# Kernel optimization log

Hardware: AMD Instinct MI355X
Metric: run time of the kernel (lower is better)

The kernel has to match this reference:

```python
import jax, jax.numpy as jnp
import numpy as np

N = 100000   # nodes
E = 100000   # hyperedges
M = 1600000  # incidences
IN_C = 128
HID = 128
OUT_C = 64
L = 2
EPS = 1e-5


def _layer_norm(x, g, b):
    m = jnp.mean(x, axis=-1, keepdims=True)
    v = jnp.mean((x - m) ** 2, axis=-1, keepdims=True)
    return (x - m) * jax.lax.rsqrt(v + EPS) * g + b


def setup_inputs() -> dict:
    key = jax.random.key(0)
    ks = jax.random.split(key, 16)
    s_in = 1.0 / np.sqrt(IN_C)
    s_h = 1.0 / np.sqrt(HID)
    return {
        "x": jax.random.normal(ks[0], (N, IN_C), jnp.float32),
        "x_e": jax.random.normal(ks[1], (E, IN_C), jnp.float32),
        "edge_index": jax.random.randint(ks[2], (2, M), 0, N, jnp.int32),
        "in_norm_g": jnp.ones((IN_C,), jnp.float32),
        "in_norm_b": jnp.zeros((IN_C,), jnp.float32),
        "in_proj_W": jax.random.normal(ks[3], (IN_C, HID), jnp.float32) * s_in,
        "in_proj_b": jnp.zeros((HID,), jnp.float32),
        "norm_g": jnp.ones((L, HID), jnp.float32),
        "norm_b": jnp.zeros((L, HID), jnp.float32),
        "conv_W": jax.random.normal(ks[4], (L, HID, HID), jnp.float32) * s_h,
        "conv_b": jnp.zeros((L, HID), jnp.float32),
        "lin_W": jax.random.normal(ks[5], (HID, OUT_C), jnp.float32) * s_h,
        "lin_b": jnp.zeros((OUT_C,), jnp.float32),
    }


def reference(x, x_e, edge_index, in_norm_g, in_norm_b, in_proj_W, in_proj_b,
              norm_g, norm_b, conv_W, conv_b, lin_W, lin_b):
    src, dst = edge_index[0], edge_index[1]  # node ids, hyperedge ids
    h = _layer_norm(x, in_norm_g, in_norm_b)
    h = jax.nn.leaky_relu(h @ in_proj_W + in_proj_b)  # dropout = identity (eval)

    # HypergraphConv degree normalizers (hyperedge_weight = 1)
    ones = jnp.ones((M,), h.dtype)
    degD = jax.ops.segment_sum(ones, src, num_segments=N)
    D = jnp.where(degD > 0, 1.0 / degD, 0.0)          # [N]
    degB = jax.ops.segment_sum(ones, dst, num_segments=E)
    B = jnp.where(degB > 0, 1.0 / degB, 0.0)          # [E]

    for i in range(L):
        hn = _layer_norm(h, norm_g[i], norm_b[i])
        xw = hn @ conv_W[i]                            # [N, HID]
        # node -> hyperedge: sum_j B[e] * xw[j]
        he = jax.ops.segment_sum(B[dst][:, None] * xw[src], dst, num_segments=E)
        # hyperedge -> node: sum_e D[n] * he[e]
        h2 = jax.ops.segment_sum(D[src][:, None] * he[dst], src, num_segments=N)
        h = jax.nn.leaky_relu(h2 + conv_b[i])

    # MinAggregation: segment-min of gathered node features per hyperedge
    agg = jax.ops.segment_min(h[src], dst, num_segments=E)  # [E, HID]
    return agg @ lin_W + lin_b                              # [E, OUT_C]
```

## Files before the change

kernel.cpp:

```cpp
#include <hip/hip_runtime.h>

#define NN 100000
#define NE 100000
#define MI 1600000
#define HID 128
#define OUTC 64
#define LSLOPE 0.01f
#define EPSV 1e-5f
#define ADJ_STRIDE 48
#define BUILD_PASSES 6
#define BUILD_WIN ((NN + BUILD_PASSES - 1) / BUILD_PASSES)

typedef unsigned short us;
typedef __attribute__((ext_vector_type(4))) unsigned short us4;
typedef __attribute__((ext_vector_type(8))) short short8;
typedef __attribute__((ext_vector_type(16))) float f32x16;

__device__ __forceinline__ float bf2f(us h) {
    return __uint_as_float(((unsigned)h) << 16);
}
__device__ __forceinline__ us f2bf(float f) {
    unsigned u = __float_as_uint(f);
    return (us)((u + 0x7FFFu + ((u >> 16) & 1u)) >> 16);
}

__global__ void build_win_kernel(const int* __restrict__ ei,
                                 int* __restrict__ cntE, int* __restrict__ cntN,
                                 int* __restrict__ adjE, int* __restrict__ adjN,
                                 int lo, int hi) {
    int m = blockIdx.x * blockDim.x + threadIdx.x;
    if (m >= MI) return;
    int s = ei[m], d = ei[MI + m];
    if (d >= lo && d < hi) {
        int p = atomicAdd(&cntE[d], 1);
        if (p < ADJ_STRIDE) adjE[d * ADJ_STRIDE + p] = s;
    }
    if (s >= lo && s < hi) {
        int p = atomicAdd(&cntN[s], 1);
        if (p < ADJ_STRIDE) adjN[s * ADJ_STRIDE + p] = d;
    }
}

__global__ void recip2_kernel(const int* __restrict__ cntE, const int* __restrict__ cntN,
                              float* __restrict__ B, float* __restrict__ D) {
    int i = blockIdx.x * blockDim.x + threadIdx.x;
    if (i < NE) {
        int d = cntE[i]; B[i] = d > 0 ? 1.0f / (float)d : 0.0f;
    } else if (i < NE + NN) {
        int j = i - NE;
        int d = cntN[j]; D[j] = d > 0 ? 1.0f / (float)d : 0.0f;
    }
}

__global__ void wprep_kernel(const float* __restrict__ in_W, const float* __restrict__ conv_W,
                             const float* __restrict__ lin_W,
                             us* __restrict__ wt_in, us* __restrict__ wt_c0,
                             us* __restrict__ wt_c1, us* __restrict__ wt_lin) {
    int idx = blockIdx.x * blockDim.x + threadIdx.x;
    if (idx < 49152) {
        int mat = idx >> 14, r = idx & 16383;
        const float* src = mat == 0 ? in_W : (mat == 1 ? conv_W : conv_W + 16384);
        us* dst = mat == 0 ? wt_in : (mat == 1 ? wt_c0 : wt_c1);
        int n = r >> 7, k = r & 127;
        dst[r] = f2bf(src[k * 128 + n]);
    } else if (idx < 57344) {
        int r = idx - 49152;
        int n = r >> 7, k = r & 127;
        float v = lin_W[k * 64 + n];
        us h = f2bf(v);
        wt_lin[r] = h;
        wt_lin[8192 + r] = f2bf(v - bf2f(h));
    }
}

template <int MODE>
__global__ __launch_bounds__(256) void gather_kernel(
    const int* __restrict__ cnt, const int* __restrict__ adj,
    const us* __restrict__ src, const float* __restrict__ scale,
    const float* __restrict__ bias, us* __restrict__ dst, int R)
{
    int g = threadIdx.x >> 5;
    int lane = threadIdx.x & 31;
    int r = blockIdx.x * 8 + g;
    if (r >= R) return;
    int n = cnt[r]; n = n < ADJ_STRIDE ? n : ADJ_STRIDE;
    const int* arow = adj + (size_t)r * ADJ_STRIDE;
    float ax, ay, az, aw;
    if (MODE == 2) { ax = ay = az = aw = INFINITY; }
    else           { ax = ay = az = aw = 0.f; }
    const us* base = src + lane * 4;
    int j = 0;
    for (; j + 7 < n; j += 8) {
        us4 v0 = *(const us4*)(base + (size_t)arow[j]     * HID);
        us4 v1 = *(const us4*)(base + (size_t)arow[j + 1] * HID);
        us4 v2 = *(const us4*)(base + (size_t)arow[j + 2] * HID);
        us4 v3 = *(const us4*)(base + (size_t)arow[j + 3] * HID);
        us4 v4 = *(const us4*)(base + (size_t)arow[j + 4] * HID);
        us4 v5 = *(const us4*)(base + (size_t)arow[j + 5] * HID);
        us4 v6 = *(const us4*)(base + (size_t)arow[j + 6] * HID);
        us4 v7 = *(const us4*)(base + (size_t)arow[j + 7] * HID);
        if (MODE == 2) {
            ax = fminf(ax, fminf(fminf(fminf(bf2f(v0.x), bf2f(v1.x)), fminf(bf2f(v2.x), bf2f(v3.x))),
                                 fminf(fminf(bf2f(v4.x), bf2f(v5.x)), fminf(bf2f(v6.x), bf2f(v7.x)))));
            ay = fminf(ay, fminf(fminf(fminf(bf2f(v0.y), bf2f(v1.y)), fminf(bf2f(v2.y), bf2f(v3.y))),
                                 fminf(fminf(bf2f(v4.y), bf2f(v5.y)), fminf(bf2f(v6.y), bf2f(v7.y)))));
            az = fminf(az, fminf(fminf(fminf(bf2f(v0.z), bf2f(v1.z)), fminf(bf2f(v2.z), bf2f(v3.z))),
                                 fminf(fminf(bf2f(v4.z), bf2f(v5.z)), fminf(bf2f(v6.z), bf2f(v7.z)))));
            aw = fminf(aw, fminf(fminf(fminf(bf2f(v0.w), bf2f(v1.w)), fminf(bf2f(v2.w), bf2f(v3.w))),
                                 fminf(fminf(bf2f(v4.w), bf2f(v5.w)), fminf(bf2f(v6.w), bf2f(v7.w)))));
        } else {
            ax += ((bf2f(v0.x) + bf2f(v1.x)) + (bf2f(v2.x) + bf2f(v3.x)))
                + ((bf2f(v4.x) + bf2f(v5.x)) + (bf2f(v6.x) + bf2f(v7.x)));
            ay += ((bf2f(v0.y) + bf2f(v1.y)) + (bf2f(v2.y) + bf2f(v3.y)))
                + ((bf2f(v4.y) + bf2f(v5.y)) + (bf2f(v6.y) + bf2f(v7.y)));
            az += ((bf2f(v0.z) + bf2f(v1.z)) + (bf2f(v2.z) + bf2f(v3.z)))
                + ((bf2f(v4.z) + bf2f(v5.z)) + (bf2f(v6.z) + bf2f(v7.z)));
            aw += ((bf2f(v0.w) + bf2f(v1.w)) + (bf2f(v2.w) + bf2f(v3.w)))
                + ((bf2f(v4.w) + bf2f(v5.w)) + (bf2f(v6.w) + bf2f(v7.w)));
        }
    }
    for (; j + 1 < n; j += 2) {
        us4 v0 = *(const us4*)(base + (size_t)arow[j]     * HID);
        us4 v1 = *(const us4*)(base + (size_t)arow[j + 1] * HID);
        if (MODE == 2) {
            ax = fminf(ax, fminf(bf2f(v0.x), bf2f(v1.x)));
            ay = fminf(ay, fminf(bf2f(v0.y), bf2f(v1.y)));
            az = fminf(az, fminf(bf2f(v0.z), bf2f(v1.z)));
            aw = fminf(aw, fminf(bf2f(v0.w), bf2f(v1.w)));
        } else {
            ax += bf2f(v0.x) + bf2f(v1.x);
            ay += bf2f(v0.y) + bf2f(v1.y);
            az += bf2f(v0.z) + bf2f(v1.z);
            aw += bf2f(v0.w) + bf2f(v1.w);
        }
    }
    if (j < n) {
        us4 v0 = *(const us4*)(base + (size_t)arow[j] * HID);
        if (MODE == 2) {
            ax = fminf(ax, bf2f(v0.x)); ay = fminf(ay, bf2f(v0.y));
            az = fminf(az, bf2f(v0.z)); aw = fminf(aw, bf2f(v0.w));
        } else {
            ax += bf2f(v0.x); ay += bf2f(v0.y); az += bf2f(v0.z); aw += bf2f(v0.w);
        }
    }
    if (MODE == 0) {
        float s = scale[r];
        ax *= s; ay *= s; az *= s; aw *= s;
    } else if (MODE == 1) {
        float s = scale[r];
        float4 b = *(const float4*)(bias + lane * 4);
        float x;
        x = s * ax + b.x; ax = x > 0.f ? x : LSLOPE * x;
        x = s * ay + b.y; ay = x > 0.f ? x : LSLOPE * x;
        x = s * az + b.z; az = x > 0.f ? x : LSLOPE * x;
        x = s * aw + b.w; aw = x > 0.f ? x : LSLOPE * x;
    }
    us4 o;
    o.x = f2bf(ax); o.y = f2bf(ay); o.z = f2bf(az); o.w = f2bf(aw);
    *(us4*)(dst + (size_t)r * HID + lane * 4) = o;
}

template <int NC, bool ABF16, bool OBF16, bool SPLIT>
__global__ __launch_bounds__(512) void mfma_gemm_kernel(
    const void* __restrict__ Av, const float* __restrict__ ln_g, const float* __restrict__ ln_b,
    const us* __restrict__ WT, const float* __restrict__ bias,
    void* __restrict__ outv, int R, int flags)
{
    constexpr int SA = 136;
    constexpr int NW = (SPLIT ? 2 : 1) * NC;
    constexpr int CT = NC / 64;
    __shared__ us As[128 * SA];
    __shared__ us Ws[NW * SA];
    __shared__ float red_s[512];
    __shared__ float red_q[512];
    __shared__ float r_mean[128];
    __shared__ float r_rstd[128];

    const int t = threadIdx.x;
    const int row0 = blockIdx.x * 128;

    constexpr int WUS4 = NW * 128 / 4;
    #pragma unroll
    for (int i = t; i < WUS4; i += 512) {
        us4 w = ((const us4*)WT)[i];
        int nrow = i >> 5, k4 = i & 31;
        *(us4*)(Ws + nrow * SA + k4 * 4) = w;
    }

    {
        const int r = t >> 2, sub = t & 3;
        const int gr = row0 + r;
        float v[32];
        if (gr < R) {
            if (ABF16) {
                const us* ap = (const us*)Av + (size_t)gr * 128 + sub * 32;
                #pragma unroll
                for (int j4 = 0; j4 < 8; ++j4) {
                    us4 x4 = *(const us4*)(ap + j4 * 4);
                    v[j4 * 4 + 0] = bf2f(x4.x); v[j4 * 4 + 1] = bf2f(x4.y);
                    v[j4 * 4 + 2] = bf2f(x4.z); v[j4 * 4 + 3] = bf2f(x4.w);
                }
            } else {
                const float* ap = (const float*)Av + (size_t)gr * 128 + sub * 32;
                #pragma unroll
                for (int j4 = 0; j4 < 8; ++j4) {
                    float4 f4 = *(const float4*)(ap + j4 * 4);
                    v[j4 * 4 + 0] = f4.x; v[j4 * 4 + 1] = f4.y;
                    v[j4 * 4 + 2] = f4.z; v[j4 * 4 + 3] = f4.w;
                }
            }
        } else {
            #pragma unroll
            for (int j = 0; j < 32; ++j) v[j] = 0.f;
        }
        if (flags & 1) {
            float s = 0.f, q = 0.f;
            #pragma unroll
            for (int j = 0; j < 32; ++j) { s += v[j]; q += v[j] * v[j]; }
            red_s[t] = s; red_q[t] = q;
            __syncthreads();
            if (t < 128) {
                float ss = red_s[t * 4] + red_s[t * 4 + 1] + red_s[t * 4 + 2] + red_s[t * 4 + 3];
                float qq = red_q[t * 4] + red_q[t * 4 + 1] + red_q[t * 4 + 2] + red_q[t * 4 + 3];
                float mu = ss * (1.0f / 128.0f);
                float var = qq * (1.0f / 128.0f) - mu * mu;
                r_mean[t] = mu;
                r_rstd[t] = rsqrtf(var + EPSV);
            }
            __syncthreads();
            float mu = r_mean[r], rs = r_rstd[r];
            #pragma unroll
            for (int j4 = 0; j4 < 8; ++j4) {
                float4 g4 = *(const float4*)(ln_g + sub * 32 + j4 * 4);
                float4 b4 = *(const float4*)(ln_b + sub * 32 + j4 * 4);
                v[j4 * 4 + 0] = (v[j4 * 4 + 0] - mu) * rs * g4.x + b4.x;
                v[j4 * 4 + 1] = (v[j4 * 4 + 1] - mu) * rs * g4.y + b4.y;
                v[j4 * 4 + 2] = (v[j4 * 4 + 2] - mu) * rs * g4.z + b4.z;
                v[j4 * 4 + 3] = (v[j4 * 4 + 3] - mu) * rs * g4.w + b4.w;
            }
        }
        #pragma unroll
        for (int j4 = 0; j4 < 8; ++j4) {
            us4 o;
            o.x = f2bf(v[j4 * 4 + 0]); o.y = f2bf(v[j4 * 4 + 1]);
            o.z = f2bf(v[j4 * 4 + 2]); o.w = f2bf(v[j4 * 4 + 3]);
            *(us4*)(As + r * SA + sub * 32 + j4 * 4) = o;
        }
    }
    __syncthreads();

    const int lane = t & 63;
    const int wave = t >> 6;
    const int wr = (wave & 3) * 32;
    const int wc = (wave >> 2) * (NC / 2);
    const int m = lane & 31;
    const int half = lane >> 5;
    const us* a_base = As + (wr + m) * SA + half * 8;

    f32x16 acc[CT];
    #pragma unroll
    for (int ct = 0; ct < CT; ++ct) acc[ct] = (f32x16)(0.0f);

    #pragma unroll
    for (int ks = 0; ks < 8; ++ks) {
        short8 a = *(const short8*)(a_base + ks * 16);
        #pragma unroll
        for (int ct = 0; ct < CT; ++ct) {
            const us* b_base = Ws + (wc + ct * 32 + m) * SA + half * 8 + ks * 16;
            short8 b = *(const short8*)b_base;
            acc[ct] = __builtin_amdgcn_mfma_f32_32x32x16_bf16(a, b, acc[ct], 0, 0, 0);
            if (SPLIT) {
                short8 bl = *(const short8*)(b_base + (size_t)NC * SA);
                acc[ct] = __builtin_amdgcn_mfma_f32_32x32x16_bf16(a, bl, acc[ct], 0, 0, 0);
            }
        }
    }

    #pragma unroll
    for (int ct = 0; ct < CT; ++ct) {
        int gc = wc + ct * 32 + m;
        float bv = bias ? bias[gc] : 0.f;
        #pragma unroll
        for (int reg = 0; reg < 16; ++reg) {
            int rloc = (reg & 3) + 8 * (reg >> 2) + 4 * half;
            int gr = row0 + wr + rloc;
            if (gr < R) {
                float y = acc[ct][reg] + bv;
                if (flags & 4) y = y > 0.f ? y : LSLOPE * y;
                if (OBF16) ((us*)outv)[(size_t)gr * NC + gc] = f2bf(y);
                else       ((float*)outv)[(size_t)gr * NC + gc] = y;
            }
        }
    }
}

extern "C" void kernel_launch(void* const* d_in, const int* in_sizes, int n_in,
                              void* d_out, int out_size, void* d_ws, size_t ws_size,
                              hipStream_t stream) {
    const float* x      = (const float*)d_in[0];
    const int*   ei     = (const int*)d_in[2];
    const float* in_g   = (const float*)d_in[3];
    const float* in_b   = (const float*)d_in[4];
    const float* in_W   = (const float*)d_in[5];
    const float* in_pb  = (const float*)d_in[6];
    const float* norm_g = (const float*)d_in[7];
    const float* norm_b = (const float*)d_in[8];
    const float* conv_W = (const float*)d_in[9];
    const float* conv_b = (const float*)d_in[10];
    const float* lin_W  = (const float*)d_in[11];
    const float* lin_b  = (const float*)d_in[12];
    float* out = (float*)d_out;

    us* h_bf   = (us*)d_ws;
    us* xw_bf  = h_bf  + (size_t)NN * HID;
    us* he_bf  = xw_bf + (size_t)NN * HID;
    us* agg_bf = he_bf + (size_t)NE * HID;
    float* D    = (float*)(agg_bf + (size_t)NE * HID);
    float* B    = D + NN;
    int* cntE   = (int*)(B + NE);
    int* cntN   = cntE + NE;
    int* adjE   = cntN + NN;
    int* adjN   = adjE + (size_t)NE * ADJ_STRIDE;
    us* wt_in  = (us*)(adjN + (size_t)NN * ADJ_STRIDE);
    us* wt_c0  = wt_in + 128 * 128;
    us* wt_c1  = wt_c0 + 128 * 128;
    us* wt_lin = wt_c1 + 128 * 128;

    hipMemsetAsync(cntE, 0, (size_t)(NN + NE) * sizeof(int), stream);
    for (int p = 0; p < BUILD_PASSES; ++p) {
        int lo = p * BUILD_WIN;
        int hi = lo + BUILD_WIN < NN ? lo + BUILD_WIN : NN;
        build_win_kernel<<<(MI + 255) / 256, 256, 0, stream>>>(ei, cntE, cntN, adjE, adjN, lo, hi);
    }
    recip2_kernel<<<(NN + NE + 255) / 256, 256, 0, stream>>>(cntE, cntN, B, D);

    wprep_kernel<<<(57344 + 255) / 256, 256, 0, stream>>>(
        in_W, conv_W, lin_W, wt_in, wt_c0, wt_c1, wt_lin);

    mfma_gemm_kernel<HID, false, true, false><<<(NN + 127) / 128, 512, 0, stream>>>(
        x, in_g, in_b, wt_in, in_pb, h_bf, NN, 1 | 4);

    for (int i = 0; i < 2; ++i) {
        mfma_gemm_kernel<HID, true, true, false><<<(NN + 127) / 128, 512, 0, stream>>>(
            h_bf, norm_g + i * HID, norm_b + i * HID, i ? wt_c1 : wt_c0,
            nullptr, xw_bf, NN, 1);
        gather_kernel<0><<<(NE + 7) / 8, 256, 0, stream>>>(cntE, adjE, xw_bf, B, nullptr, he_bf, NE);
        gather_kernel<1><<<(NN + 7) / 8, 256, 0, stream>>>(cntN, adjN, he_bf, D, conv_b + i * HID, h_bf, NN);
    }

    gather_kernel<2><<<(NE + 7) / 8, 256, 0, stream>>>(cntE, adjE, h_bf, nullptr, nullptr, agg_bf, NE);

    mfma_gemm_kernel<OUTC, true, false, true><<<(NE + 127) / 128, 512, 0, stream>>>(
        agg_bf, nullptr, nullptr, wt_lin, lin_b, out, NE, 0);
}
```

Baseline: 757.8 us.

## Widen gather loads to 16 bytes and fold build passes into one launch

Gather kernels now use 16 lanes per row, each loading 8 bf16 values (16 bytes) per neighbour instead of 4. This halves the number of load instructions and doubles the rows handled per block. The windowed adjacency build goes from 6 separate launches to one grid covering 10 windows, and the reciprocal-degree and weight-prep kernels are merged into one launch. Running all windows in a single grid loses the ordering between windows, which may raise atomic contention and weaken the locality that windowing was meant to give.

After: 745.8 us (median of 2 runs). Within noise of the previous version (-1.6%).

```diff
diff --git a/kernel.cpp b/kernel.cpp
--- a/kernel.cpp
+++ b/kernel.cpp
@@ -8,11 +8,13 @@
 #define LSLOPE 0.01f
 #define EPSV 1e-5f
 #define ADJ_STRIDE 48
-#define BUILD_PASSES 6
+#define BUILD_PASSES 10
 #define BUILD_WIN ((NN + BUILD_PASSES - 1) / BUILD_PASSES)
+#define BUILD_NB ((MI + 255) / 256)
 
 typedef unsigned short us;
 typedef __attribute__((ext_vector_type(4))) unsigned short us4;
+typedef __attribute__((ext_vector_type(8))) unsigned short us8;
 typedef __attribute__((ext_vector_type(8))) short short8;
 typedef __attribute__((ext_vector_type(16))) float f32x16;
 
@@ -24,12 +26,14 @@
     return (us)((u + 0x7FFFu + ((u >> 16) & 1u)) >> 16);
 }
 
-__global__ void build_win_kernel(const int* __restrict__ ei,
+__global__ void build_all_kernel(const int* __restrict__ ei,
                                  int* __restrict__ cntE, int* __restrict__ cntN,
-                                 int* __restrict__ adjE, int* __restrict__ adjN,
-                                 int lo, int hi) {
-    int m = blockIdx.x * blockDim.x + threadIdx.x;
+                                 int* __restrict__ adjE, int* __restrict__ adjN) {
+    int pass = blockIdx.x / BUILD_NB;
+    int m = (blockIdx.x - pass * BUILD_NB) * 256 + threadIdx.x;
     if (m >= MI) return;
+    int lo = pass * BUILD_WIN;
+    int hi = lo + BUILD_WIN < NN ? lo + BUILD_WIN : NN;
     int s = ei[m], d = ei[MI + m];
     if (d >= lo && d < hi) {
         int p = atomicAdd(&cntE[d], 1);
@@ -41,35 +45,34 @@
     }
 }
 
-__global__ void recip2_kernel(const int* __restrict__ cntE, const int* __restrict__ cntN,
-                              float* __restrict__ B, float* __restrict__ D) {
+__global__ void prep_kernel(const int* __restrict__ cntE, const int* __restrict__ cntN,
+                            float* __restrict__ B, float* __restrict__ D,
+                            const float* __restrict__ in_W, const float* __restrict__ conv_W,
+                            const float* __restrict__ lin_W,
+                            us* __restrict__ wt_in, us* __restrict__ wt_c0,
+                            us* __restrict__ wt_c1, us* __restrict__ wt_lin) {
     int i = blockIdx.x * blockDim.x + threadIdx.x;
     if (i < NE) {
         int d = cntE[i]; B[i] = d > 0 ? 1.0f / (float)d : 0.0f;
     } else if (i < NE + NN) {
         int j = i - NE;
         int d = cntN[j]; D[j] = d > 0 ? 1.0f / (float)d : 0.0f;
-    }
-}
-
-__global__ void wprep_kernel(const float* __restrict__ in_W, const float* __restrict__ conv_W,
-                             const float* __restrict__ lin_W,
-                             us* __restrict__ wt_in, us* __restrict__ wt_c0,
-                             us* __restrict__ wt_c1, us* __restrict__ wt_lin) {
-    int idx = blockIdx.x * blockDim.x + threadIdx.x;
-    if (idx < 49152) {
-        int mat = idx >> 14, r = idx & 16383;
-        const float* src = mat == 0 ? in_W : (mat == 1 ? conv_W : conv_W + 16384);
-        us* dst = mat == 0 ? wt_in : (mat == 1 ? wt_c0 : wt_c1);
-        int n = r >> 7, k = r & 127;
-        dst[r] = f2bf(src[k * 128 + n]);
-    } else if (idx < 57344) {
-        int r = idx - 49152;
-        int n = r >> 7, k = r & 127;
-        float v = lin_W[k * 64 + n];
-        us h = f2bf(v);
-        wt_lin[r] = h;
-        wt_lin[8192 + r] = f2bf(v - bf2f(h));
+    } else {
+        int idx = i - (NE + NN);
+        if (idx < 49152) {
+            int mat = idx >> 14, r = idx & 16383;
+            const float* src = mat == 0 ? in_W : (mat == 1 ? conv_W : conv_W + 16384);
+            us* dst = mat == 0 ? wt_in : (mat == 1 ? wt_c0 : wt_c1);
+            int n = r >> 7, k = r & 127;
+            dst[r] = f2bf(src[k * 128 + n]);
+        } else if (idx < 57344) {
+            int r = idx - 49152;
+            int n = r >> 7, k = r & 127;
+            float v = lin_W[k * 64 + n];
+            us h = f2bf(v);
+            wt_lin[r] = h;
+            wt_lin[8192 + r] = f2bf(v - bf2f(h));
+        }
     }
 }
 
@@ -79,85 +82,58 @@
     const us* __restrict__ src, const float* __restrict__ scale,
     const float* __restrict__ bias, us* __restrict__ dst, int R)
 {
-    int g = threadIdx.x >> 5;
-    int lane = threadIdx.x & 31;
-    int r = blockIdx.x * 8 + g;
+    const int q = threadIdx.x >> 4;
+    const int lane = threadIdx.x & 15;
+    const int r = blockIdx.x * 16 + q;
     if (r >= R) return;
     int n = cnt[r]; n = n < ADJ_STRIDE ? n : ADJ_STRIDE;
     const int* arow = adj + (size_t)r * ADJ_STRIDE;
-    float ax, ay, az, aw;
-    if (MODE == 2) { ax = ay = az = aw = INFINITY; }
-    else           { ax = ay = az = aw = 0.f; }
-    const us* base = src + lane * 4;
+    float a[8];
+    #pragma unroll
+    for (int k = 0; k < 8; ++k) a[k] = (MODE == 2) ? INFINITY : 0.f;
+    const us* base = src + lane * 8;
     int j = 0;
     for (; j + 7 < n; j += 8) {
-        us4 v0 = *(const us4*)(base + (size_t)arow[j]     * HID);
-        us4 v1 = *(const us4*)(base + (size_t)arow[j + 1] * HID);
-        us4 v2 = *(const us4*)(base + (size_t)arow[j + 2] * HID);
-        us4 v3 = *(const us4*)(base + (size_t)arow[j + 3] * HID);
-        us4 v4 = *(const us4*)(base + (size_t)arow[j + 4] * HID);
-        us4 v5 = *(const us4*)(base + (size_t)arow[j + 5] * HID);
-        us4 v6 = *(const us4*)(base + (size_t)arow[j + 6] * HID);
-        us4 v7 = *(const us4*)(base + (size_t)arow[j + 7] * HID);
-        if (MODE == 2) {
-            ax = fminf(ax, fminf(fminf(fminf(bf2f(v0.x), bf2f(v1.x)), fminf(bf2f(v2.x), bf2f(v3.x))),
-                                 fminf(fminf(bf2f(v4.x), bf2f(v5.x)), fminf(bf2f(v6.x), bf2f(v7.x)))));
-            ay = fminf(ay, fminf(fminf(fminf(bf2f(v0.y), bf2f(v1.y)), fminf(bf2f(v2.y), bf2f(v3.y))),
-                                 fminf(fminf(bf2f(v4.y), bf2f(v5.y)), fminf(bf2f(v6.y), bf2f(v7.y)))));
-            az = fminf(az, fminf(fminf(fminf(bf2f(v0.z), bf2f(v1.z)), fminf(bf2f(v2.z), bf2f(v3.z))),
-                                 fminf(fminf(bf2f(v4.z), bf2f(v5.z)), fminf(bf2f(v6.z), bf2f(v7.z)))));
-            aw = fminf(aw, fminf(fminf(fminf(bf2f(v0.w), bf2f(v1.w)), fminf(bf2f(v2.w), bf2f(v3.w))),
-                                 fminf(fminf(bf2f(v4.w), bf2f(v5.w)), fminf(bf2f(v6.w), bf2f(v7.w)))));
-        } else {
-            ax += ((bf2f(v0.x) + bf2f(v1.x)) + (bf2f(v2.x) + bf2f(v3.x)))
-                + ((bf2f(v4.x) + bf2f(v5.x)) + (bf2f(v6.x) + bf2f(v7.x)));
-            ay += ((bf2f(v0.y) + bf2f(v1.y)) + (bf2f(v2.y) + bf2f(v3.y)))
-                + ((bf2f(v4.y) + bf2f(v5.y)) + (bf2f(v6.y) + bf2f(v7.y)));
-            az += ((bf2f(v0.z) + bf2f(v1.z)) + (bf2f(v2.z) + bf2f(v3.z)))
-                + ((bf2f(v4.z) + bf2f(v5.z)) + (bf2f(v6.z) + bf2f(v7.z)));
-            aw += ((bf2f(v0.w) + bf2f(v1.w)) + (bf2f(v2.w) + bf2f(v3.w)))
-                + ((bf2f(v4.w) + bf2f(v5.w)) + (bf2f(v6.w) + bf2f(v7.w)));
-        }
-    }
-    for (; j + 1 < n; j += 2) {
-        us4 v0 = *(const us4*)(base + (size_t)arow[j]     * HID);
-        us4 v1 = *(const us4*)(base + (size_t)arow[j + 1] * HID);
-        if (MODE == 2) {
-            ax = fminf(ax, fminf(bf2f(v0.x), bf2f(v1.x)));
-            ay = fminf(ay, fminf(bf2f(v0.y), bf2f(v1.y)));
-            az = fminf(az, fminf(bf2f(v0.z), bf2f(v1.z)));
-            aw = fminf(aw, fminf(bf2f(v0.w), bf2f(v1.w)));
-        } else {
-            ax += bf2f(v0.x) + bf2f(v1.x);
-            ay += bf2f(v0.y) + bf2f(v1.y);
-            az += bf2f(v0.z) + bf2f(v1.z);
-            aw += bf2f(v0.w) + bf2f(v1.w);
-        }
-    }
-    if (j < n) {
-        us4 v0 = *(const us4*)(base + (size_t)arow[j] * HID);
-        if (MODE == 2) {
-            ax = fminf(ax, bf2f(v0.x)); ay = fminf(ay, bf2f(v0.y));
-            az = fminf(az, bf2f(v0.z)); aw = fminf(aw, bf2f(v0.w));
-        } else {
-            ax += bf2f(v0.x); ay += bf2f(v0.y); az += bf2f(v0.z); aw += bf2f(v0.w);
+        us8 v[8];
+        #pragma unroll
+        for (int u = 0; u < 8; ++u)
+            v[u] = *(const us8*)(base + (size_t)arow[j + u] * HID);
+        #pragma unroll
+        for (int u = 0; u < 8; ++u) {
+            #pragma unroll
+            for (int k = 0; k < 8; ++k) {
+                float f = bf2f(v[u][k]);
+                a[k] = (MODE == 2) ? fminf(a[k], f) : (a[k] + f);
+            }
+        }
+    }
+    for (; j < n; ++j) {
+        us8 v = *(const us8*)(base + (size_t)arow[j] * HID);
+        #pragma unroll
+        for (int k = 0; k < 8; ++k) {
+            float f = bf2f(v[k]);
+            a[k] = (MODE == 2) ? fminf(a[k], f) : (a[k] + f);
         }
     }
     if (MODE == 0) {
         float s = scale[r];
-        ax *= s; ay *= s; az *= s; aw *= s;
+        #pragma unroll
+        for (int k = 0; k < 8; ++k) a[k] *= s;
     } else if (MODE == 1) {
         float s = scale[r];
-        float4 b = *(const float4*)(bias + lane * 4);
-        float x;
-        x = s * ax + b.x; ax = x > 0.f ? x : LSLOPE * x;
-        x = s * ay + b.y; ay = x > 0.f ? x : LSLOPE * x;
-        x = s * az + b.z; az = x > 0.f ? x : LSLOPE * x;
-        x = s * aw + b.w; aw = x > 0.f ? x : LSLOPE * x;
-    }
-    us4 o;
-    o.x = f2bf(ax); o.y = f2bf(ay); o.z = f2bf(az); o.w = f2bf(aw);
-    *(us4*)(dst + (size_t)r * HID + lane * 4) = o;
+        float4 b0 = *(const float4*)(bias + lane * 8);
+        float4 b1 = *(const float4*)(bias + lane * 8 + 4);
+        float bb[8] = {b0.x, b0.y, b0.z, b0.w, b1.x, b1.y, b1.z, b1.w};
+        #pragma unroll
+        for (int k = 0; k < 8; ++k) {
+            float x = s * a[k] + bb[k];
+            a[k] = x > 0.f ? x : LSLOPE * x;
+        }
+    }
+    us8 o;
+    #pragma unroll
+    for (int k = 0; k < 8; ++k) o[k] = f2bf(a[k]);
+    *(us8*)(dst + (size_t)r * HID + lane * 8) = o;
 }
 
 template <int NC, bool ABF16, bool OBF16, bool SPLIT>
@@ -327,15 +303,10 @@
     us* wt_lin = wt_c1 + 128 * 128;
 
     hipMemsetAsync(cntE, 0, (size_t)(NN + NE) * sizeof(int), stream);
-    for (int p = 0; p < BUILD_PASSES; ++p) {
-        int lo = p * BUILD_WIN;
-        int hi = lo + BUILD_WIN < NN ? lo + BUILD_WIN : NN;
-        build_win_kernel<<<(MI + 255) / 256, 256, 0, stream>>>(ei, cntE, cntN, adjE, adjN, lo, hi);
-    }
-    recip2_kernel<<<(NN + NE + 255) / 256, 256, 0, stream>>>(cntE, cntN, B, D);
-
-    wprep_kernel<<<(57344 + 255) / 256, 256, 0, stream>>>(
-        in_W, conv_W, lin_W, wt_in, wt_c0, wt_c1, wt_lin);
+    build_all_kernel<<<BUILD_PASSES * BUILD_NB, 256, 0, stream>>>(ei, cntE, cntN, adjE, adjN);
+
+    prep_kernel<<<(NE + NN + 57344 + 255) / 256, 256, 0, stream>>>(
+        cntE, cntN, B, D, in_W, conv_W, lin_W, wt_in, wt_c0, wt_c1, wt_lin);
 
     mfma_gemm_kernel<HID, false, true, false><<<(NN + 127) / 128, 512, 0, stream>>>(
         x, in_g, in_b, wt_in, in_pb, h_bf, NN, 1 | 4);
@@ -344,11 +315,11 @@
         mfma_gemm_kernel<HID, true, true, false><<<(NN + 127) / 128, 512, 0, stream>>>(
             h_bf, norm_g + i * HID, norm_b + i * HID, i ? wt_c1 : wt_c0,
             nullptr, xw_bf, NN, 1);
-        gather_kernel<0><<<(NE + 7) / 8, 256, 0, stream>>>(cntE, adjE, xw_bf, B, nullptr, he_bf, NE);
-        gather_kernel<1><<<(NN + 7) / 8, 256, 0, stream>>>(cntN, adjN, he_bf, D, conv_b + i * HID, h_bf, NN);
-    }
-
-    gather_kernel<2><<<(NE + 7) / 8, 256, 0, stream>>>(cntE, adjE, h_bf, nullptr, nullptr, agg_bf, NE);
+        gather_kernel<0><<<(NE + 15) / 16, 256, 0, stream>>>(cntE, adjE, xw_bf, B, nullptr, he_bf, NE);
+        gather_kernel<1><<<(NN + 15) / 16, 256, 0, stream>>>(cntN, adjN, he_bf, D, conv_b + i * HID, h_bf, NN);
+    }
+
+    gather_kernel<2><<<(NE + 15) / 16, 256, 0, stream>>>(cntE, adjE, h_bf, nullptr, nullptr, agg_bf, NE);
 
     mfma_gemm_kernel<OUTC, true, false, true><<<(NE + 127) / 128, 512, 0, stream>>>(
         agg_bf, nullptr, nullptr, wt_lin, lin_b, out, NE, 0);
```
